# Performance work log

Measured on AMD Instinct MI355X. Metric: run time of the kernel, lower is better.

The kernel has to match this reference:

```python
import jax, jax.numpy as jnp
import numpy as np

NUM_HEADS = 12
H_PATCH = 14
W_PATCH = 14
ROPE_BASE = 10000.0


def _rope_2d(head_dim):
    # 2D RoPE: first half of head_dim encodes row (h), second half encodes col (w).
    half = head_dim // 2
    inv_freq = 1.0 / (ROPE_BASE ** (jnp.arange(0, half, 2, dtype=jnp.float32) / half))  # [half/2]
    ys = jnp.arange(H_PATCH)
    xs = jnp.arange(W_PATCH)
    yy, xx = jnp.meshgrid(ys, xs, indexing='ij')
    h_idx = yy.reshape(-1).astype(jnp.float32)  # [N]
    w_idx = xx.reshape(-1).astype(jnp.float32)  # [N]
    freqs_h = h_idx[:, None] * inv_freq[None, :]  # [N, half/2]
    freqs_w = w_idx[:, None] * inv_freq[None, :]  # [N, half/2]
    emb = jnp.concatenate([freqs_h, freqs_w], axis=-1)  # [N, half]
    emb = jnp.concatenate([emb, emb], axis=-1)          # [N, head_dim]
    return jnp.cos(emb), jnp.sin(emb)


def _rotate_half(x):
    d = x.shape[-1] // 2
    return jnp.concatenate([-x[..., d:], x[..., :d]], axis=-1)


def reference(x, qkv_w, qkv_b, proj_w, proj_b):
    BxT, N, C = x.shape
    hd = C // NUM_HEADS
    qkv = x @ qkv_w.T + qkv_b                                    # [BxT, N, 3C]
    qkv = qkv.reshape(BxT, N, 3, NUM_HEADS, hd)
    qkv = jnp.transpose(qkv, (2, 0, 3, 1, 4))                    # [3, BxT, H, N, hd]
    q, k, v = qkv[0], qkv[1], qkv[2]
    cos, sin = _rope_2d(hd)                                      # [N, hd]
    cos = cos[None, None, :, :]
    sin = sin[None, None, :, :]
    q = q * cos + _rotate_half(q) * sin
    k = k * cos + _rotate_half(k) * sin
    scale = hd ** -0.5
    attn = jnp.einsum('bhqd,bhkd->bhqk', q, k) * scale           # [BxT, H, N, N]
    attn = jax.nn.softmax(attn, axis=-1)
    out = jnp.einsum('bhqk,bhkd->bhqd', attn, v)                 # [BxT, H, N, hd]
    out = jnp.transpose(out, (0, 2, 1, 3)).reshape(BxT, N, C)
    out = out @ proj_w.T + proj_b
    return out


def setup_inputs() -> dict:
    key = jax.random.key(0)
    ks = jax.random.split(key, 5)
    C = 768
    return {
        'x': jax.random.normal(ks[0], (128, 196, C), dtype=jnp.float32),
        'qkv_w': jax.random.normal(ks[1], (3 * C, C), dtype=jnp.float32) * (C ** -0.5),
        'qkv_b': jax.random.normal(ks[2], (3 * C,), dtype=jnp.float32) * 0.02,
        'proj_w': jax.random.normal(ks[3], (C, C), dtype=jnp.float32) * (C ** -0.5),
        'proj_b': jax.random.normal(ks[4], (C,), dtype=jnp.float32) * 0.02,
    }
```

## Files before the change

### kernel.cpp

```cpp
#include <hip/hip_runtime.h>
#include <hip/hip_bf16.h>

typedef __attribute__((ext_vector_type(8))) short short8;
typedef __attribute__((ext_vector_type(4))) float f32x4;

#define GLD16(gp, lp) \
  __builtin_amdgcn_global_load_lds((const __attribute__((address_space(1))) void*)(gp), \
                                   (__attribute__((address_space(3))) void*)(lp), 16, 0, 0)

__device__ __forceinline__ f32x4 mfma_bf16(short8 a, short8 b, f32x4 c) {
  return __builtin_amdgcn_mfma_f32_16x16x32_bf16(a, b, c, 0, 0, 0);
}

__global__ __launch_bounds__(256) void prep_kernel(
    const float* __restrict__ x, const float* __restrict__ qkv_w,
    const float* __restrict__ proj_w, __hip_bfloat16* __restrict__ xb,
    __hip_bfloat16* __restrict__ w1b, __hip_bfloat16* __restrict__ w2b,
    float* __restrict__ cosT, float* __restrict__ sinT) {
  const int N1 = 25088 * 768 / 4;
  const int N2 = 2304 * 768 / 4;
  const int N3 = 768 * 768 / 4;
  int i = blockIdx.x * 256 + threadIdx.x;
  const float* src;
  __hip_bfloat16* dst;
  int idx;
  if (i < N1) {
    src = x; dst = xb; idx = i;
  } else if (i < N1 + N2) {
    src = qkv_w; dst = w1b; idx = i - N1;
  } else if (i < N1 + N2 + N3) {
    src = proj_w; dst = w2b; idx = i - N1 - N2;
  } else {
    int r = i - (N1 + N2 + N3);
    if (r < 196 * 64) {
      int t = r >> 6, d = r & 63;
      int c = d & 31;
      float pos = (c < 16) ? (float)(t / 14) : (float)(t % 14);
      int j = c & 15;
      float invf = expf(-(float)j * 0.5756462732485114f);
      float ang = pos * invf;
      cosT[r] = cosf(ang);
      sinT[r] = sinf(ang);
    }
    return;
  }
  float4 v = reinterpret_cast<const float4*>(src)[idx];
  ushort4 o;
  o.x = __builtin_bit_cast(unsigned short, __float2bfloat16(v.x));
  o.y = __builtin_bit_cast(unsigned short, __float2bfloat16(v.y));
  o.z = __builtin_bit_cast(unsigned short, __float2bfloat16(v.z));
  o.w = __builtin_bit_cast(unsigned short, __float2bfloat16(v.w));
  reinterpret_cast<ushort4*>(dst)[idx] = o;
}

__global__ __launch_bounds__(256) void gemm_qkv_kernel(
    const __hip_bfloat16* __restrict__ A, const __hip_bfloat16* __restrict__ W,
    const float* __restrict__ bias, const float* __restrict__ cosT,
    const float* __restrict__ sinT, __hip_bfloat16* __restrict__ qb,
    __hip_bfloat16* __restrict__ kb, __hip_bfloat16* __restrict__ vb) {
  __shared__ __align__(16) __hip_bfloat16 As[128 * 64];
  __shared__ __align__(16) __hip_bfloat16 Bs[128 * 64];
  const int tid = threadIdx.x;
  const int id = blockIdx.x;
  const int sup = id / 72, rem = id % 72;
  const int bm = sup * 4 + rem / 18;
  const int bn = rem % 18;
  const int lane = tid & 63, wv = tid >> 6;
  const int wm = wv >> 1, wn = wv & 1;
  const int quad = lane >> 4, ln = lane & 15;

  const int r0 = tid >> 3;
  const int csw = ((tid & 7) ^ (r0 & 7)) * 8;
  const __hip_bfloat16* Ag = A + ((long)(bm * 128 + r0) * 768 + csw);
  const __hip_bfloat16* Wg = W + ((long)(bn * 128 + r0) * 768 + csw);
  __hip_bfloat16* As0 = As + tid * 8;
  __hip_bfloat16* Bs0 = Bs + tid * 8;

  const int c0 = (quad ^ (ln & 7)) * 8;
  const int c1 = c0 ^ 32;

  f32x4 acc[4][4];
#pragma unroll
  for (int i = 0; i < 4; i++)
#pragma unroll
    for (int j = 0; j < 4; j++) acc[i][j] = (f32x4){0.f, 0.f, 0.f, 0.f};

  for (int k0 = 0; k0 < 768; k0 += 64) {
    GLD16(Ag + k0,            As0);
    GLD16(Ag + 32 * 768 + k0, As0 + 2048);
    GLD16(Ag + 64 * 768 + k0, As0 + 4096);
    GLD16(Ag + 96 * 768 + k0, As0 + 6144);
    GLD16(Wg + k0,            Bs0);
    GLD16(Wg + 32 * 768 + k0, Bs0 + 2048);
    GLD16(Wg + 64 * 768 + k0, Bs0 + 4096);
    GLD16(Wg + 96 * 768 + k0, Bs0 + 6144);
    __syncthreads();
#pragma unroll
    for (int kk = 0; kk < 2; kk++) {
      const int cc = kk ? c1 : c0;
      short8 af[4], bf[4];
#pragma unroll
      for (int i = 0; i < 4; i++)
        af[i] = *(const short8*)(As + (wm * 64 + i * 16 + ln) * 64 + cc);
#pragma unroll
      for (int j = 0; j < 4; j++)
        bf[j] = *(const short8*)(Bs + (wn * 64 + j * 16 + ln) * 64 + cc);
#pragma unroll
      for (int i = 0; i < 4; i++)
#pragma unroll
        for (int j = 0; j < 4; j++) acc[i][j] = mfma_bf16(af[i], bf[j], acc[i][j]);
    }
    __syncthreads();
  }

  const int ncolbase = bn * 128 + wn * 64;
  const int s = ncolbase / 768;
  const int hh = (ncolbase % 768) >> 6;
  __hip_bfloat16* outb = (s == 0) ? qb : ((s == 1) ? kb : vb);
  float bi[4];
#pragma unroll
  for (int j = 0; j < 4; j++) bi[j] = bias[ncolbase + j * 16 + ln];
  const bool dorope = (s < 2);

#pragma unroll
  for (int i = 0; i < 4; i++) {
#pragma unroll
    for (int r = 0; r < 4; r++) {
      int m = bm * 128 + wm * 64 + i * 16 + quad * 4 + r;
      int b = m / 196, t = m - b * 196;
      float v0 = acc[i][0][r] + bi[0];
      float v1 = acc[i][1][r] + bi[1];
      float v2 = acc[i][2][r] + bi[2];
      float v3 = acc[i][3][r] + bi[3];
      if (dorope) {
        const float* ct = cosT + t * 64 + ln;
        const float* st = sinT + t * 64 + ln;
        float c0f = ct[0], c1f = ct[16], c2f = ct[32], c3f = ct[48];
        float s0 = st[0], s1 = st[16], s2 = st[32], s3 = st[48];
        float w0 = v0 * c0f - v2 * s0;
        float w1 = v1 * c1f - v3 * s1;
        float w2 = v2 * c2f + v0 * s2;
        float w3 = v3 * c3f + v1 * s3;
        v0 = w0; v1 = w1; v2 = w2; v3 = w3;
      }
      __hip_bfloat16* op = outb + ((long)(b * 12 + hh) * 196 + t) * 64 + ln;
      op[0]  = __float2bfloat16(v0);
      op[16] = __float2bfloat16(v1);
      op[32] = __float2bfloat16(v2);
      op[48] = __float2bfloat16(v3);
    }
  }
}

__global__ __launch_bounds__(256) void attn_kernel(
    const __hip_bfloat16* __restrict__ qb, const __hip_bfloat16* __restrict__ kb,
    const __hip_bfloat16* __restrict__ vb, __hip_bfloat16* __restrict__ att) {
  __shared__ __align__(16) __hip_bfloat16 Vt[64 * 232];
  __shared__ __align__(16) __hip_bfloat16 Ps[4][16 * 232];
  const int bh = blockIdx.x;
  const int b = bh / 12, h = bh - b * 12;
  const int tid = threadIdx.x;
  const int lane = tid & 63, wv = tid >> 6;
  const int quad = lane >> 4, ln = lane & 15;
  const __hip_bfloat16* qg = qb + (long)bh * (196 * 64);
  const __hip_bfloat16* kg = kb + (long)bh * (196 * 64);
  const __hip_bfloat16* vg = vb + (long)bh * (196 * 64);

  for (int ch = tid; ch < 224 * 8; ch += 256) {
    int row = ch >> 3, c = (ch & 7) * 8;
    unsigned short vals[8] = {0, 0, 0, 0, 0, 0, 0, 0};
    if (row < 196) *(uint4*)vals = *(const uint4*)(vg + row * 64 + c);
#pragma unroll
    for (int u = 0; u < 8; u++)
      ((unsigned short*)Vt)[(c + u) * 232 + row] = vals[u];
  }

  __hip_bfloat16* Pw = &Ps[wv][0];
#pragma unroll
  for (int r = 0; r < 4; r++)
    Pw[(quad * 4 + r) * 232 + 208 + ln] = __float2bfloat16(0.f);
  __syncthreads();

  for (int qt = wv; qt < 13; qt += 4) {
    int tok = qt * 16 + ln;
    if (tok > 195) tok = 195;
    short8 aq0 = *(const short8*)(qg + tok * 64 + quad * 8);
    short8 aq1 = *(const short8*)(qg + tok * 64 + 32 + quad * 8);

    f32x4 sacc[13];
#pragma unroll
    for (int ct = 0; ct < 13; ct++) {
      int krow = ct * 16 + ln;
      if (krow > 195) krow = 195;
      const __hip_bfloat16* kp = kg + krow * 64 + quad * 8;
      short8 b0 = *(const short8*)kp;
      short8 b1 = *(const short8*)(kp + 32);
      f32x4 cacc = (f32x4){0.f, 0.f, 0.f, 0.f};
      cacc = mfma_bf16(aq0, b0, cacc);
      cacc = mfma_bf16(aq1, b1, cacc);
      sacc[ct] = cacc;
    }

    float sm[4] = {0.f, 0.f, 0.f, 0.f};
#pragma unroll
    for (int ct = 0; ct < 13; ct++) {
      bool valid = (ct * 16 + ln) < 196;
#pragma unroll
      for (int r = 0; r < 4; r++) {
        float p = valid ? __expf(sacc[ct][r] * 0.125f) : 0.f;
        sm[r] += p;
        Pw[(quad * 4 + r) * 232 + ct * 16 + ln] = __float2bfloat16(p);
      }
    }
#pragma unroll
    for (int mk = 1; mk < 16; mk <<= 1) {
#pragma unroll
      for (int r = 0; r < 4; r++) sm[r] += __shfl_xor(sm[r], mk, 64);
    }
    asm volatile("" ::: "memory");

    f32x4 o[4];
#pragma unroll
    for (int j = 0; j < 4; j++) o[j] = (f32x4){0.f, 0.f, 0.f, 0.f};
#pragma unroll
    for (int kt = 0; kt < 7; kt++) {
      short8 pa = *(const short8*)(Pw + ln * 232 + kt * 32 + quad * 8);
#pragma unroll
      for (int j = 0; j < 4; j++) {
        short8 bv = *(const short8*)(Vt + (j * 16 + ln) * 232 + kt * 32 + quad * 8);
        o[j] = mfma_bf16(pa, bv, o[j]);
      }
    }
    asm volatile("" ::: "memory");

    float rl[4];
#pragma unroll
    for (int r = 0; r < 4; r++) rl[r] = 1.0f / sm[r];
    int trow = qt * 16 + quad * 4;
#pragma unroll
    for (int r = 0; r < 4; r++) {
      int t = trow + r;
      if (t < 196) {
        __hip_bfloat16* op = att + (long)(b * 196 + t) * 768 + h * 64 + ln;
#pragma unroll
        for (int j = 0; j < 4; j++) op[j * 16] = __float2bfloat16(o[j][r] * rl[r]);
      }
    }
  }
}

__global__ __launch_bounds__(256) void gemm_proj_kernel(
    const __hip_bfloat16* __restrict__ A, const __hip_bfloat16* __restrict__ W,
    const float* __restrict__ bias, float* __restrict__ out) {
  __shared__ __align__(16) __hip_bfloat16 As[128 * 64];
  __shared__ __align__(16) __hip_bfloat16 Bs[128 * 64];
  const int tid = threadIdx.x;
  const int id = blockIdx.x;
  const int sup = id / 24, rem = id % 24;
  const int bm = sup * 4 + rem / 6;
  const int bn = rem % 6;
  const int lane = tid & 63, wv = tid >> 6;
  const int wm = wv >> 1, wn = wv & 1;
  const int quad = lane >> 4, ln = lane & 15;

  const int r0 = tid >> 3;
  const int csw = ((tid & 7) ^ (r0 & 7)) * 8;
  const __hip_bfloat16* Ag = A + ((long)(bm * 128 + r0) * 768 + csw);
  const __hip_bfloat16* Wg = W + ((long)(bn * 128 + r0) * 768 + csw);
  __hip_bfloat16* As0 = As + tid * 8;
  __hip_bfloat16* Bs0 = Bs + tid * 8;

  const int c0 = (quad ^ (ln & 7)) * 8;
  const int c1 = c0 ^ 32;

  f32x4 acc[4][4];
#pragma unroll
  for (int i = 0; i < 4; i++)
#pragma unroll
    for (int j = 0; j < 4; j++) acc[i][j] = (f32x4){0.f, 0.f, 0.f, 0.f};

  for (int k0 = 0; k0 < 768; k0 += 64) {
    GLD16(Ag + k0,            As0);
    GLD16(Ag + 32 * 768 + k0, As0 + 2048);
    GLD16(Ag + 64 * 768 + k0, As0 + 4096);
    GLD16(Ag + 96 * 768 + k0, As0 + 6144);
    GLD16(Wg + k0,            Bs0);
    GLD16(Wg + 32 * 768 + k0, Bs0 + 2048);
    GLD16(Wg + 64 * 768 + k0, Bs0 + 4096);
    GLD16(Wg + 96 * 768 + k0, Bs0 + 6144);
    __syncthreads();
#pragma unroll
    for (int kk = 0; kk < 2; kk++) {
      const int cc = kk ? c1 : c0;
      short8 af[4], bf[4];
#pragma unroll
      for (int i = 0; i < 4; i++)
        af[i] = *(const short8*)(As + (wm * 64 + i * 16 + ln) * 64 + cc);
#pragma unroll
      for (int j = 0; j < 4; j++)
        bf[j] = *(const short8*)(Bs + (wn * 64 + j * 16 + ln) * 64 + cc);
#pragma unroll
      for (int i = 0; i < 4; i++)
#pragma unroll
        for (int j = 0; j < 4; j++) acc[i][j] = mfma_bf16(af[i], bf[j], acc[i][j]);
    }
    __syncthreads();
  }

  const int ncolbase = bn * 128 + wn * 64;
  float bi[4];
#pragma unroll
  for (int j = 0; j < 4; j++) bi[j] = bias[ncolbase + j * 16 + ln];
#pragma unroll
  for (int i = 0; i < 4; i++) {
#pragma unroll
    for (int r = 0; r < 4; r++) {
      int m = bm * 128 + wm * 64 + i * 16 + quad * 4 + r;
      float* op = out + (long)m * 768 + ncolbase + ln;
      op[0]  = acc[i][0][r] + bi[0];
      op[16] = acc[i][1][r] + bi[1];
      op[32] = acc[i][2][r] + bi[2];
      op[48] = acc[i][3][r] + bi[3];
    }
  }
}

extern "C" void kernel_launch(void* const* d_in, const int* in_sizes, int n_in,
                              void* d_out, int out_size, void* d_ws, size_t ws_size,
                              hipStream_t stream) {
  const float* x      = (const float*)d_in[0];
  const float* qkv_w  = (const float*)d_in[1];
  const float* qkv_b  = (const float*)d_in[2];
  const float* proj_w = (const float*)d_in[3];
  const float* proj_b = (const float*)d_in[4];
  float* out = (float*)d_out;
  (void)in_sizes; (void)n_in; (void)out_size; (void)ws_size;

  char* ws = (char*)d_ws;
  size_t off = 0;
  auto alloc = [&](size_t bytes) -> void* {
    void* p = (void*)(ws + off);
    off += (bytes + 255) & ~(size_t)255;
    return p;
  };
  const size_t MB0 = (size_t)25088 * 768 * 2;
  __hip_bfloat16* xb   = (__hip_bfloat16*)alloc(MB0);
  __hip_bfloat16* w1b  = (__hip_bfloat16*)alloc((size_t)2304 * 768 * 2);
  __hip_bfloat16* w2b  = (__hip_bfloat16*)alloc((size_t)768 * 768 * 2);
  float* cosT          = (float*)alloc(196 * 64 * 4);
  float* sinT          = (float*)alloc(196 * 64 * 4);
  __hip_bfloat16* qbuf = (__hip_bfloat16*)alloc(MB0);
  __hip_bfloat16* kbuf = (__hip_bfloat16*)alloc(MB0);
  __hip_bfloat16* vbuf = (__hip_bfloat16*)alloc(MB0);
  __hip_bfloat16* attb = xb;

  prep_kernel<<<21169, 256, 0, stream>>>(x, qkv_w, proj_w, xb, w1b, w2b, cosT, sinT);
  gemm_qkv_kernel<<<3528, 256, 0, stream>>>(xb, w1b, qkv_b, cosT, sinT,
                                            qbuf, kbuf, vbuf);
  attn_kernel<<<1536, 256, 0, stream>>>(qbuf, kbuf, vbuf, attb);
  gemm_proj_kernel<<<1176, 256, 0, stream>>>(attb, w2b, proj_b, out);
}
```

Measured before the change: 386.0 us.

## Stream attention P through small per-wave LDS chunks and raise occupancy

The attention kernel no longer writes the full 16x208 probability row to LDS before the PV MFMAs. It now processes 32-key chunks, staging only a 16x32 tile per wave and running the PV MFMA right after each chunk's exp. This shrinks the LDS footprint, and launch_bounds(256,4) asks for four blocks per CU. The V transpose store also rotates its write order per thread to reduce LDS bank conflicts. In exchange there are more LDS round trips and compiler barriers per chunk, and the register cap may cause spills.

After: 454.4 us. +17.7%, slower.

```diff
diff --git a/kernel.cpp b/kernel.cpp
--- a/kernel.cpp
+++ b/kernel.cpp
@@ -152,11 +152,11 @@
   }
 }
 
-__global__ __launch_bounds__(256) void attn_kernel(
+__global__ __launch_bounds__(256, 4) void attn_kernel(
     const __hip_bfloat16* __restrict__ qb, const __hip_bfloat16* __restrict__ kb,
     const __hip_bfloat16* __restrict__ vb, __hip_bfloat16* __restrict__ att) {
   __shared__ __align__(16) __hip_bfloat16 Vt[64 * 232];
-  __shared__ __align__(16) __hip_bfloat16 Ps[4][16 * 232];
+  __shared__ __align__(16) __hip_bfloat16 Ps[4][16 * 40];
   const int bh = blockIdx.x;
   const int b = bh / 12, h = bh - b * 12;
   const int tid = threadIdx.x;
@@ -167,19 +167,18 @@
   const __hip_bfloat16* vg = vb + (long)bh * (196 * 64);
 
   for (int ch = tid; ch < 224 * 8; ch += 256) {
-    int row = ch >> 3, c = (ch & 7) * 8;
+    int row = ch >> 3, cq = ch & 7, c = cq * 8;
     unsigned short vals[8] = {0, 0, 0, 0, 0, 0, 0, 0};
     if (row < 196) *(uint4*)vals = *(const uint4*)(vg + row * 64 + c);
 #pragma unroll
-    for (int u = 0; u < 8; u++)
+    for (int uu = 0; uu < 8; uu++) {
+      int u = (uu + cq) & 7;
       ((unsigned short*)Vt)[(c + u) * 232 + row] = vals[u];
-  }
+    }
+  }
+  __syncthreads();
 
   __hip_bfloat16* Pw = &Ps[wv][0];
-#pragma unroll
-  for (int r = 0; r < 4; r++)
-    Pw[(quad * 4 + r) * 232 + 208 + ln] = __float2bfloat16(0.f);
-  __syncthreads();
 
   for (int qt = wv; qt < 13; qt += 4) {
     int tok = qt * 16 + ln;
@@ -202,36 +201,54 @@
     }
 
     float sm[4] = {0.f, 0.f, 0.f, 0.f};
-#pragma unroll
-    for (int ct = 0; ct < 13; ct++) {
-      bool valid = (ct * 16 + ln) < 196;
+    f32x4 o[4];
+#pragma unroll
+    for (int j = 0; j < 4; j++) o[j] = (f32x4){0.f, 0.f, 0.f, 0.f};
+
+#pragma unroll
+    for (int g = 0; g < 6; g++) {
+#pragma unroll
+      for (int h2 = 0; h2 < 2; h2++) {
+        int ct = 2 * g + h2;
+#pragma unroll
+        for (int r = 0; r < 4; r++) {
+          float p = __expf(sacc[ct][r] * 0.125f);
+          sm[r] += p;
+          Pw[(quad * 4 + r) * 40 + h2 * 16 + ln] = __float2bfloat16(p);
+        }
+      }
+      asm volatile("" ::: "memory");
+      short8 pa = *(const short8*)(Pw + ln * 40 + quad * 8);
+#pragma unroll
+      for (int j = 0; j < 4; j++) {
+        short8 bv = *(const short8*)(Vt + (j * 16 + ln) * 232 + g * 32 + quad * 8);
+        o[j] = mfma_bf16(pa, bv, o[j]);
+      }
+      asm volatile("" ::: "memory");
+    }
+    {
 #pragma unroll
       for (int r = 0; r < 4; r++) {
-        float p = valid ? __expf(sacc[ct][r] * 0.125f) : 0.f;
+        float p = (ln < 4) ? __expf(sacc[12][r] * 0.125f) : 0.f;
         sm[r] += p;
-        Pw[(quad * 4 + r) * 232 + ct * 16 + ln] = __float2bfloat16(p);
-      }
-    }
+        Pw[(quad * 4 + r) * 40 + ln] = __float2bfloat16(p);
+        Pw[(quad * 4 + r) * 40 + 16 + ln] = __float2bfloat16(0.f);
+      }
+      asm volatile("" ::: "memory");
+      short8 pa = *(const short8*)(Pw + ln * 40 + quad * 8);
+#pragma unroll
+      for (int j = 0; j < 4; j++) {
+        short8 bv = *(const short8*)(Vt + (j * 16 + ln) * 232 + 192 + quad * 8);
+        o[j] = mfma_bf16(pa, bv, o[j]);
+      }
+      asm volatile("" ::: "memory");
+    }
+
 #pragma unroll
     for (int mk = 1; mk < 16; mk <<= 1) {
 #pragma unroll
       for (int r = 0; r < 4; r++) sm[r] += __shfl_xor(sm[r], mk, 64);
     }
-    asm volatile("" ::: "memory");
-
-    f32x4 o[4];
-#pragma unroll
-    for (int j = 0; j < 4; j++) o[j] = (f32x4){0.f, 0.f, 0.f, 0.f};
-#pragma unroll
-    for (int kt = 0; kt < 7; kt++) {
-      short8 pa = *(const short8*)(Pw + ln * 232 + kt * 32 + quad * 8);
-#pragma unroll
-      for (int j = 0; j < 4; j++) {
-        short8 bv = *(const short8*)(Vt + (j * 16 + ln) * 232 + kt * 32 + quad * 8);
-        o[j] = mfma_bf16(pa, bv, o[j]);
-      }
-    }
-    asm volatile("" ::: "memory");
 
     float rl[4];
 #pragma unroll
```
